# Optimization experiments

Hardware: AMD Instinct MI355X
Metric: run time of the kernel (lower is better)

## Reference

```python
import jax, jax.numpy as jnp
import numpy as np
import math

D_MODEL = 512
N_TOTAL = 1024
HW = 4096
EPSILON = 0.2
NUM_HEADS = 8
D_K = D_MODEL // NUM_HEADS
BATCH = 4


def setup_inputs() -> dict:
    rng = jax.random.key(0)
    ks = jax.random.split(rng, 16)
    s = 1.0 / math.sqrt(D_MODEL)
    inp = {
        "query": jax.random.normal(ks[0], (BATCH, N_TOTAL, D_MODEL), jnp.float32),
        "key": jax.random.normal(ks[1], (BATCH, HW, D_MODEL), jnp.float32),
        "value": jax.random.normal(ks[2], (BATCH, HW, D_MODEL), jnp.float32),
        "x_tilde": jax.random.uniform(ks[3], (HW, 2), jnp.float32),
        "x_hat": jax.random.uniform(ks[4], (N_TOTAL, HW, 2), jnp.float32),
        # torch nn.Linear params: W is (out, in), y = x @ W.T + b
        "Wq": jax.random.uniform(ks[5], (D_MODEL, D_MODEL), jnp.float32, -s, s),
        "bq": jax.random.uniform(ks[6], (D_MODEL,), jnp.float32, -s, s),
        "Wk": jax.random.uniform(ks[7], (D_MODEL, D_MODEL), jnp.float32, -s, s),
        "bk": jax.random.uniform(ks[8], (D_MODEL,), jnp.float32, -s, s),
        "Wv": jax.random.uniform(ks[9], (D_MODEL, D_MODEL), jnp.float32, -s, s),
        "bv": jax.random.uniform(ks[10], (D_MODEL,), jnp.float32, -s, s),
        "Wo": jax.random.uniform(ks[11], (D_MODEL, D_MODEL), jnp.float32, -s, s),
        "bo": jax.random.uniform(ks[12], (D_MODEL,), jnp.float32, -s, s),
    }
    return inp


def _geo_mask(x_tilde, x_hat):
    # x_tilde: (HW, 2), x_hat: (N_total, HW, 2)
    diff = x_tilde[None, :, :] - x_hat            # (N, HW, 2)
    dist = jnp.sqrt(jnp.sum(diff * diff, axis=-1))  # (N, HW)
    return jnp.where(dist < EPSILON, 0.0, -jnp.inf).astype(x_hat.dtype)


def reference(query, key, value, x_tilde, x_hat, Wq, bq, Wk, bk, Wv, bv, Wo, bo):
    B = query.shape[0]
    M_geo = _geo_mask(x_tilde, x_hat)  # (N, HW)

    def heads(x, W, b):
        y = x @ W.T + b                                   # (B, L, D)
        return y.reshape(B, -1, NUM_HEADS, D_K).transpose(0, 2, 1, 3)  # (B, H, L, dk)

    Q = heads(query, Wq, bq)   # (B, H, N, dk)
    K = heads(key, Wk, bk)     # (B, H, HW, dk)
    V = heads(value, Wv, bv)   # (B, H, HW, dk)

    scores = jnp.einsum("bhnd,bhmd->bhnm", Q, K) / math.sqrt(D_K)
    scores = scores + M_geo[None, None, :, :]
    attn = jax.nn.softmax(scores, axis=-1)                # (B, H, N, HW)
    ctx = jnp.einsum("bhnm,bhmd->bhnd", attn, V)          # (B, H, N, dk)
    ctx = ctx.transpose(0, 2, 1, 3).reshape(B, -1, D_MODEL)
    out = ctx @ Wo.T + bo                                 # (B, N, D)
    return out, attn
```

## Files before the change

### kernel.cpp

```cpp
#include <hip/hip_runtime.h>
#include <cstdint>
#include <cstddef>

typedef __attribute__((ext_vector_type(4))) float f32x4;
typedef __attribute__((ext_vector_type(8))) _Float16 h16x8;
typedef __attribute__((ext_vector_type(2))) _Float16 h16x2;
typedef __attribute__((ext_vector_type(8))) short s16x8;
typedef __attribute__((ext_vector_type(4))) short s16x4;
typedef unsigned short u16;
typedef unsigned long long u64;

static __device__ inline u16 f2h(float f) {
    _Float16 h = (_Float16)f;
    return __builtin_bit_cast(u16, h);
}

static __device__ inline f32x4 mfma16(h16x8 a, h16x8 b, f32x4 c) {
    return __builtin_amdgcn_mfma_f32_16x16x32_f16(a, b, c, 0, 0, 0);
}

static __device__ inline float redsum16(float v) {
    v += __shfl_xor(v, 1);
    v += __shfl_xor(v, 2);
    v += __shfl_xor(v, 4);
    v += __shfl_xor(v, 8);
    return v;
}

__global__ __launch_bounds__(256) void cvt_h_kernel(const float* __restrict__ src,
                                                    u16* __restrict__ dst, float scale) {
    int i = (blockIdx.x * 256 + threadIdx.x) * 4;
    f32x4 v = *(const f32x4*)(src + i);
    s16x4 o;
    o[0] = (short)f2h(v[0] * scale); o[1] = (short)f2h(v[1] * scale);
    o[2] = (short)f2h(v[2] * scale); o[3] = (short)f2h(v[3] * scale);
    *(s16x4*)(dst + i) = o;
}

__global__ __launch_bounds__(256) void mask_kernel(const float* __restrict__ xt,
                                                   const float* __restrict__ xh,
                                                   u64* __restrict__ mb) {
    int tid  = threadIdx.x;
    int lane = tid & 63;
    int wv   = blockIdx.x * 4 + (tid >> 6);
    int n    = wv >> 6;
    int mbk  = wv & 63;
    int m    = (mbk << 6) + lane;
    size_t hidx = ((size_t)n * 4096 + m) * 2;
    float dx = xt[2 * m]     - xh[hidx];
    float dy = xt[2 * m + 1] - xh[hidx + 1];
    bool p = sqrtf(dx * dx + dy * dy) < 0.2f;
    u64 bal = __ballot(p);
    if (lane == 0) mb[wv] = bal;
}

template <int INF32, int MODE, int LSHIFT>
__global__ __launch_bounds__(256) void proj_kernel(const void* __restrict__ Xv,
                                                   const u16* __restrict__ Wb,
                                                   const float* __restrict__ bias,
                                                   float bscale,
                                                   void* __restrict__ Yv) {
    __shared__ u16 aT[128 * 72];
    __shared__ u16 bT[128 * 72];

    int tid  = threadIdx.x;
    int lane = tid & 63, w = tid >> 6, q = lane >> 4, m15 = lane & 15;
    int wm = w >> 1, wn = w & 1;
    int m0 = blockIdx.x * 128, n0 = blockIdx.y * 128;
    int sRow = tid >> 1, sC = (tid & 1) * 32;

    f32x4 acc[4][4];
#pragma unroll
    for (int i = 0; i < 4; ++i)
#pragma unroll
        for (int j = 0; j < 4; ++j) { f32x4 z = {0.f, 0.f, 0.f, 0.f}; acc[i][j] = z; }

    for (int kb = 0; kb < 512; kb += 64) {
        if (INF32) {
            const float* X = (const float*)Xv;
#pragma unroll
            for (int j = 0; j < 8; ++j) {
                int col = sC + j * 4;
                f32x4 v = *(const f32x4*)(X + (size_t)(m0 + sRow) * 512 + kb + col);
                s16x4 o;
                o[0] = (short)f2h(v[0]); o[1] = (short)f2h(v[1]);
                o[2] = (short)f2h(v[2]); o[3] = (short)f2h(v[3]);
                *(s16x4*)(aT + sRow * 72 + col) = o;
            }
        } else {
            const u16* X = (const u16*)Xv;
#pragma unroll
            for (int j = 0; j < 4; ++j) {
                int col = sC + j * 8;
                s16x8 v = *(const s16x8*)(X + (size_t)(m0 + sRow) * 512 + kb + col);
                *(s16x8*)(aT + sRow * 72 + col) = v;
            }
        }
#pragma unroll
        for (int j = 0; j < 4; ++j) {
            int col = sC + j * 8;
            s16x8 v = *(const s16x8*)(Wb + (size_t)(n0 + sRow) * 512 + kb + col);
            *(s16x8*)(bT + sRow * 72 + col) = v;
        }
        __syncthreads();
#pragma unroll
        for (int kk = 0; kk < 2; ++kk) {
            h16x8 af[4], bf[4];
#pragma unroll
            for (int t = 0; t < 4; ++t) {
                af[t] = *(const h16x8*)(aT + (wm * 64 + t * 16 + m15) * 72 + kk * 32 + q * 8);
                bf[t] = *(const h16x8*)(bT + (wn * 64 + t * 16 + m15) * 72 + kk * 32 + q * 8);
            }
#pragma unroll
            for (int am = 0; am < 4; ++am)
#pragma unroll
                for (int bn = 0; bn < 4; ++bn)
                    acc[am][bn] = mfma16(af[am], bf[bn], acc[am][bn]);
        }
        __syncthreads();
    }

#pragma unroll
    for (int am = 0; am < 4; ++am) {
        int mg = m0 + wm * 64 + am * 16 + q * 4;
#pragma unroll
        for (int bn = 0; bn < 4; ++bn) {
            int col = n0 + wn * 64 + bn * 16 + m15;
            float bv = bias[col] * bscale;
            if (MODE == 2) {
                float* Y = (float*)Yv;
#pragma unroll
                for (int r = 0; r < 4; ++r)
                    Y[(size_t)(mg + r) * 512 + col] = acc[am][bn][r] + bv;
            } else if (MODE == 3) {
                u16* Y = (u16*)Yv;
                int hh = col >> 6, d = col & 63;
#pragma unroll
                for (int r = 0; r < 4; ++r) {
                    int m = mg + r;
                    int bb = m >> LSHIFT;
                    int nn = m & ((1 << LSHIFT) - 1);
                    Y[(((size_t)(bb * 8 + hh) << LSHIFT) + nn) * 64 + d] = f2h(acc[am][bn][r] + bv);
                }
            } else {
                u16* Yt = (u16*)Yv;
                int bidx = mg >> 12, hw0 = mg & 4095;
                int hh = col >> 6, d = col & 63;
                s16x4 o;
#pragma unroll
                for (int r = 0; r < 4; ++r) o[r] = (short)f2h(acc[am][bn][r] + bv);
                *(s16x4*)(Yt + ((size_t)((bidx << 3) + hh) * 64 + d) * 4096 + hw0) = o;
            }
        }
    }
}

__global__ __launch_bounds__(512) void attn_kernel(const u16* __restrict__ Qh,
                                                   const u16* __restrict__ Kh,
                                                   const u16* __restrict__ Vt,
                                                   const u64* __restrict__ mbits,
                                                   float* __restrict__ attnO,
                                                   u16* __restrict__ ctxO) {
    __shared__ u64   smask[1024];
    __shared__ float sred[8][16];
    __shared__ float srowi[16];
    __shared__ u16   sps[8][16 * 72];
    __shared__ float sctx[1024];

    int tid  = threadIdx.x;
    int lane = tid & 63, w = tid >> 6, q = lane >> 4, m15 = lane & 15;
    int i = blockIdx.x;
    int jj = i >> 3;
    int bh = (i & 7) * 4 + (jj & 3);
    int n0 = (jj >> 2) * 16;
    int b = bh >> 3, h = bh & 7;

    for (int t = tid; t < 1024; t += 512) {
        smask[t] = mbits[(size_t)n0 * 64 + t];
        sctx[t]  = 0.f;
    }
    __syncthreads();

    h16x8 aQ[2];
    {
        const u16* Qp = Qh + (((size_t)bh << 10) + n0 + m15) * 64 + q * 8;
        aQ[0] = *(const h16x8*)(Qp);
        aQ[1] = *(const h16x8*)(Qp + 32);
    }

    const u16* Kp = Kh + (((size_t)bh << 12) + (w << 9) + m15) * 64 + q * 8;
    const float L2E = 1.44269504f;

    unsigned st[8][8];
    float ls[4] = {0.f, 0.f, 0.f, 0.f};
#pragma unroll
    for (int cc = 0; cc < 8; ++cc) {
        int widx = w * 8 + cc;
        u64 mk[4];
#pragma unroll
        for (int r = 0; r < 4; ++r) mk[r] = smask[(q * 4 + r) * 64 + widx];
#pragma unroll
        for (int tt = 0; tt < 4; ++tt) {
            const u16* kp = Kp + (size_t)(cc * 4 + tt) * (16 * 64);
            h16x8 b0 = *(const h16x8*)(kp);
            h16x8 b1 = *(const h16x8*)(kp + 32);
            f32x4 z = {0.f, 0.f, 0.f, 0.f};
            f32x4 c0 = mfma16(aQ[0], b0, mfma16(aQ[1], b1, z));
            int bit = tt * 16 + m15;
            float p[4];
#pragma unroll
            for (int r = 0; r < 4; ++r) {
                p[r] = ((mk[r] >> bit) & 1ull) ? exp2f(c0[r] * L2E) : 0.f;
                ls[r] += p[r];
            }
            st[cc][tt * 2 + 0] = __builtin_bit_cast(unsigned, __builtin_amdgcn_cvt_pkrtz(p[0], p[1]));
            st[cc][tt * 2 + 1] = __builtin_bit_cast(unsigned, __builtin_amdgcn_cvt_pkrtz(p[2], p[3]));
        }
    }
#pragma unroll
    for (int r = 0; r < 4; ++r) {
        float v = redsum16(ls[r]);
        if (m15 == 0) sred[w][q * 4 + r] = v;
    }
    __syncthreads();
    if (tid < 16) {
        float ss = 0.f;
#pragma unroll
        for (int ww = 0; ww < 8; ++ww) ss += sred[ww][tid];
        srowi[tid] = 1.0f / ss;
    }
    __syncthreads();
    float iv[4];
#pragma unroll
    for (int r = 0; r < 4; ++r) iv[r] = srowi[q * 4 + r];

    const u16* Vp = Vt + (((size_t)bh << 6) + m15) * 4096 + (w << 9) + q * 8;
    float* aBp = attnO + (((size_t)bh << 10) + n0 + q * 4) * 4096 + (w << 9) + m15;

    f32x4 ctxa[4];
#pragma unroll
    for (int dt = 0; dt < 4; ++dt) { f32x4 z = {0.f, 0.f, 0.f, 0.f}; ctxa[dt] = z; }

#pragma unroll
    for (int cc = 0; cc < 8; ++cc) {
#pragma unroll
        for (int tt = 0; tt < 4; ++tt) {
#pragma unroll
            for (int j = 0; j < 2; ++j) {
                unsigned u = st[cc][tt * 2 + j];
                sps[w][(q * 4 + j * 2 + 0) * 72 + tt * 16 + m15] = (u16)(u & 0xffffu);
                sps[w][(q * 4 + j * 2 + 1) * 72 + tt * 16 + m15] = (u16)(u >> 16);
                h16x2 hv = __builtin_bit_cast(h16x2, u);
                float f0 = (float)hv[0] * iv[j * 2 + 0];
                float f1 = (float)hv[1] * iv[j * 2 + 1];
                __builtin_nontemporal_store(f0, aBp + (size_t)(j * 2 + 0) * 4096 + cc * 64 + tt * 16);
                __builtin_nontemporal_store(f1, aBp + (size_t)(j * 2 + 1) * 4096 + cc * 64 + tt * 16);
            }
        }
#pragma unroll
        for (int half = 0; half < 2; ++half) {
            h16x8 aP = *(const h16x8*)(&sps[w][m15 * 72 + half * 32 + q * 8]);
#pragma unroll
            for (int dt = 0; dt < 4; ++dt) {
                h16x8 bV = *(const h16x8*)(Vp + (size_t)dt * (16 * 4096) + cc * 64 + half * 32);
                ctxa[dt] = mfma16(aP, bV, ctxa[dt]);
            }
        }
    }

#pragma unroll
    for (int dt = 0; dt < 4; ++dt)
#pragma unroll
        for (int r = 0; r < 4; ++r)
            atomicAdd(&sctx[(q * 4 + r) * 64 + dt * 16 + m15], ctxa[dt][r] * iv[r]);
    __syncthreads();
    for (int t = tid; t < 1024; t += 512) {
        int rr = t >> 6, d = t & 63;
        ctxO[(((size_t)b << 10) + n0 + rr) * 512 + h * 64 + d] = f2h(sctx[t]);
    }
}

extern "C" void kernel_launch(void* const* d_in, const int* in_sizes, int n_in,
                              void* d_out, int out_size, void* d_ws, size_t ws_size,
                              hipStream_t stream) {
    (void)in_sizes; (void)n_in; (void)out_size; (void)ws_size;
    const float* query = (const float*)d_in[0];
    const float* key   = (const float*)d_in[1];
    const float* value = (const float*)d_in[2];
    const float* x_tilde = (const float*)d_in[3];
    const float* x_hat   = (const float*)d_in[4];
    const float* Wq = (const float*)d_in[5];  const float* bq = (const float*)d_in[6];
    const float* Wk = (const float*)d_in[7];  const float* bk = (const float*)d_in[8];
    const float* Wv = (const float*)d_in[9];  const float* bv = (const float*)d_in[10];
    const float* Wo = (const float*)d_in[11]; const float* bo = (const float*)d_in[12];

    char* ws = (char*)d_ws;
    u16* wq   = (u16*)(ws + 0);
    u16* wk   = (u16*)(ws + 524288);
    u16* wv   = (u16*)(ws + 1048576);
    u16* wo   = (u16*)(ws + 1572864);
    u16* Qh   = (u16*)(ws + 2097152);
    u16* Kh   = (u16*)(ws + 6291456);
    u16* Vtb  = (u16*)(ws + 23068672);
    u16* ctxb = (u16*)(ws + 39845888);
    u64* mbits = (u64*)(ws + 44040192);

    cvt_h_kernel<<<256, 256, 0, stream>>>(Wq, wq, 0.125f);
    cvt_h_kernel<<<256, 256, 0, stream>>>(Wk, wk, 1.0f);
    cvt_h_kernel<<<256, 256, 0, stream>>>(Wv, wv, 1.0f);
    cvt_h_kernel<<<256, 256, 0, stream>>>(Wo, wo, 1.0f);
    mask_kernel<<<16384, 256, 0, stream>>>(x_tilde, x_hat, mbits);

    proj_kernel<1, 3, 10><<<dim3(32, 4),  256, 0, stream>>>(query, wq, bq, 0.125f, Qh);
    proj_kernel<1, 3, 12><<<dim3(128, 4), 256, 0, stream>>>(key,   wk, bk, 1.0f,   Kh);
    proj_kernel<1, 1, 12><<<dim3(128, 4), 256, 0, stream>>>(value, wv, bv, 1.0f,   Vtb);

    float* attnO = (float*)d_out + 2097152;
    attn_kernel<<<2048, 512, 0, stream>>>(Qh, Kh, Vtb, mbits, attnO, ctxb);

    proj_kernel<0, 2, 10><<<dim3(32, 4), 256, 0, stream>>>(ctxb, wo, bo, 1.0f, d_out);
}
```

Before: 985.9 us.

## Stage full probability tile in LDS and write attn with 16-byte vector stores

Drops the per-wave register array of packed probabilities and the small per-wave LDS staging buffer. Instead the whole 16x4096 fp16 probability tile goes into a roughly 128KB LDS buffer during the score pass. The second pass reads that buffer both as the MFMA A operand and to emit the normalized attention matrix as 16-byte float4 nontemporal stores. The aim is fewer, wider global stores for the large attn output and lower register pressure from the unrolled st array. In exchange the kernel needs a very large LDS allocation, which limits occupancy to one block per CU, and the loops are no longer unrolled.

Result: faster. 947.1 us (-3.9%).

```diff
diff --git a/kernel.cpp b/kernel.cpp
--- a/kernel.cpp
+++ b/kernel.cpp
@@ -4,7 +4,7 @@
 
 typedef __attribute__((ext_vector_type(4))) float f32x4;
 typedef __attribute__((ext_vector_type(8))) _Float16 h16x8;
-typedef __attribute__((ext_vector_type(2))) _Float16 h16x2;
+typedef __attribute__((ext_vector_type(4))) _Float16 h16x4;
 typedef __attribute__((ext_vector_type(8))) short s16x8;
 typedef __attribute__((ext_vector_type(4))) short s16x4;
 typedef unsigned short u16;
@@ -161,10 +161,10 @@
                                                    const u64* __restrict__ mbits,
                                                    float* __restrict__ attnO,
                                                    u16* __restrict__ ctxO) {
+    __shared__ u16   P[16][4104];
     __shared__ u64   smask[1024];
     __shared__ float sred[8][16];
     __shared__ float srowi[16];
-    __shared__ u16   sps[8][16 * 72];
     __shared__ float sctx[1024];
 
     int tid  = threadIdx.x;
@@ -191,9 +191,7 @@
     const u16* Kp = Kh + (((size_t)bh << 12) + (w << 9) + m15) * 64 + q * 8;
     const float L2E = 1.44269504f;
 
-    unsigned st[8][8];
     float ls[4] = {0.f, 0.f, 0.f, 0.f};
-#pragma unroll
     for (int cc = 0; cc < 8; ++cc) {
         int widx = w * 8 + cc;
         u64 mk[4];
@@ -206,15 +204,14 @@
             h16x8 b1 = *(const h16x8*)(kp + 32);
             f32x4 z = {0.f, 0.f, 0.f, 0.f};
             f32x4 c0 = mfma16(aQ[0], b0, mfma16(aQ[1], b1, z));
+            int col = (w << 9) + cc * 64 + tt * 16 + m15;
             int bit = tt * 16 + m15;
-            float p[4];
 #pragma unroll
             for (int r = 0; r < 4; ++r) {
-                p[r] = ((mk[r] >> bit) & 1ull) ? exp2f(c0[r] * L2E) : 0.f;
-                ls[r] += p[r];
-            }
-            st[cc][tt * 2 + 0] = __builtin_bit_cast(unsigned, __builtin_amdgcn_cvt_pkrtz(p[0], p[1]));
-            st[cc][tt * 2 + 1] = __builtin_bit_cast(unsigned, __builtin_amdgcn_cvt_pkrtz(p[2], p[3]));
+                float p = ((mk[r] >> bit) & 1ull) ? exp2f(c0[r] * L2E) : 0.f;
+                ls[r] += p;
+                P[q * 4 + r][col] = f2h(p);
+            }
         }
     }
 #pragma unroll
@@ -231,40 +228,41 @@
     }
     __syncthreads();
     float iv[4];
-#pragma unroll
-    for (int r = 0; r < 4; ++r) iv[r] = srowi[q * 4 + r];
+    float ivr[4];
+#pragma unroll
+    for (int r = 0; r < 4; ++r) {
+        iv[r]  = srowi[q * 4 + r];
+        ivr[r] = srowi[r * 4 + q];
+    }
 
     const u16* Vp = Vt + (((size_t)bh << 6) + m15) * 4096 + (w << 9) + q * 8;
-    float* aBp = attnO + (((size_t)bh << 10) + n0 + q * 4) * 4096 + (w << 9) + m15;
+    int c0l = m15 * 4;
 
     f32x4 ctxa[4];
 #pragma unroll
     for (int dt = 0; dt < 4; ++dt) { f32x4 z = {0.f, 0.f, 0.f, 0.f}; ctxa[dt] = z; }
 
-#pragma unroll
     for (int cc = 0; cc < 8; ++cc) {
 #pragma unroll
-        for (int tt = 0; tt < 4; ++tt) {
-#pragma unroll
-            for (int j = 0; j < 2; ++j) {
-                unsigned u = st[cc][tt * 2 + j];
-                sps[w][(q * 4 + j * 2 + 0) * 72 + tt * 16 + m15] = (u16)(u & 0xffffu);
-                sps[w][(q * 4 + j * 2 + 1) * 72 + tt * 16 + m15] = (u16)(u >> 16);
-                h16x2 hv = __builtin_bit_cast(h16x2, u);
-                float f0 = (float)hv[0] * iv[j * 2 + 0];
-                float f1 = (float)hv[1] * iv[j * 2 + 1];
-                __builtin_nontemporal_store(f0, aBp + (size_t)(j * 2 + 0) * 4096 + cc * 64 + tt * 16);
-                __builtin_nontemporal_store(f1, aBp + (size_t)(j * 2 + 1) * 4096 + cc * 64 + tt * 16);
-            }
-        }
-#pragma unroll
         for (int half = 0; half < 2; ++half) {
-            h16x8 aP = *(const h16x8*)(&sps[w][m15 * 72 + half * 32 + q * 8]);
+            h16x8 aP = *(const h16x8*)(&P[m15][(w << 9) + cc * 64 + half * 32 + q * 8]);
 #pragma unroll
             for (int dt = 0; dt < 4; ++dt) {
                 h16x8 bV = *(const h16x8*)(Vp + (size_t)dt * (16 * 4096) + cc * 64 + half * 32);
                 ctxa[dt] = mfma16(aP, bV, ctxa[dt]);
             }
+        }
+        float* bp = attnO + (((size_t)bh << 10) + n0) * 4096 + (w << 9) + cc * 64 + c0l;
+#pragma unroll
+        for (int s = 0; s < 4; ++s) {
+            int row = s * 4 + q;
+            h16x4 hv = *(const h16x4*)(&P[row][(w << 9) + cc * 64 + c0l]);
+            f32x4 o;
+            o[0] = (float)hv[0] * ivr[s];
+            o[1] = (float)hv[1] * ivr[s];
+            o[2] = (float)hv[2] * ivr[s];
+            o[3] = (float)hv[3] * ivr[s];
+            __builtin_nontemporal_store(o, (f32x4*)(bp + (size_t)row * 4096));
         }
     }
 
```
